# Optimization experiments

Hardware: AMD Instinct MI355X
Metric: run time of the kernel (lower is better)

## Reference

```python
import jax, jax.numpy as jnp
import numpy as np
from jax import lax

UNITS = [100, 80, 50, 30]
IN_FEAT = 64

def setup_inputs() -> dict:
    key = jax.random.key(0)
    ks = jax.random.split(key, 16)
    B, T, F = 512, 512, IN_FEAT
    ins = [F] + UNITS[:-1]
    d = {"x": jax.random.normal(ks[0], (B, T, F), jnp.float32)}
    for li, (u, fi) in enumerate(zip(UNITS, ins)):
        din = u + fi  # concat([h, x]) per the cell
        scale = 1.0 / np.sqrt(din)
        d[f"W{li}"] = jax.random.normal(ks[1 + li], (din, 4 * u), jnp.float32) * scale
        d[f"b{li}"] = jnp.zeros((4 * u,), jnp.float32)
    d["Wout"] = jax.random.normal(ks[10], (UNITS[-1], 1), jnp.float32) * (1.0 / np.sqrt(UNITS[-1]))
    d["bout"] = jnp.zeros((1,), jnp.float32)
    return d

def _lstm_layer(x, W, b, units, return_sequences):
    # x: [B, T, F] -> hidden sequence [B, T, units] or last hidden [B, units]
    B = x.shape[0]
    h0 = jnp.zeros((B, units), x.dtype)
    c0 = jnp.zeros((B, units), x.dtype)

    def step(carry, xt):
        h, c = carry
        z = jnp.concatenate([h, xt], axis=-1) @ W + b  # [B, 4u]
        f, i, g, o = jnp.split(z, 4, axis=-1)  # gate order: forget, input, candidate, output
        f = jax.nn.sigmoid(f)
        i = jax.nn.sigmoid(i)
        g = jnp.tanh(g)
        c_new = f * c + i * g
        h_new = jax.nn.sigmoid(o) * jnp.tanh(c_new)
        return (h_new, c_new), (h_new if return_sequences else None)

    xs = jnp.swapaxes(x, 0, 1)  # [T, B, F]
    (h_last, _), hs = lax.scan(step, (h0, c0), xs)
    if return_sequences:
        return jnp.swapaxes(hs, 0, 1)  # [B, T, units]
    return h_last

def reference(x, W0, b0, W1, b1, W2, b2, W3, b3, Wout, bout):
    # Dropout layers are identity at inference (training=False).
    h = _lstm_layer(x, W0, b0, UNITS[0], True)
    h = _lstm_layer(h, W1, b1, UNITS[1], True)
    h = _lstm_layer(h, W2, b2, UNITS[2], True)
    h = _lstm_layer(h, W3, b3, UNITS[3], False)  # last-layer RNN returns final hidden only
    return h @ Wout + bout  # [B, 1]
```

## Files before the change

### kernel.cpp

```cpp
#include <hip/hip_runtime.h>


#define T_SEQ 512
#define B_TOT 512

__device__ __forceinline__ float sigmoidf_(float x) {
    return 1.0f / (1.0f + __expf(-x));
}
__device__ __forceinline__ float tanh_fast(float x) {
    float e = __expf(2.0f * x);
    return 1.0f - 2.0f / (1.0f + e);
}

template<int U, int FI, int S, int JT, int BLOCK, int WEU, bool SEQ, bool FINAL>
__global__ __launch_bounds__(BLOCK, WEU)
void lstm_layer(const float* __restrict__ X,
                const float* __restrict__ W,
                const float* __restrict__ Bv,
                float* __restrict__ Hout,
                const float* __restrict__ Wd,
                const float* __restrict__ bd,
                float* __restrict__ OUT)
{
    constexpr int DIN  = U + FI;
    constexpr int DIN4 = ((DIN + 4*S - 1) / (4*S)) * (4*S);
    constexpr int KH   = DIN4 / S;
    constexpr int G    = 4 * U;
    constexpr int NP   = G / JT;
    constexpr int NT   = NP * S;

    __shared__ __align__(16) float in0[DIN4];
    __shared__ __align__(16) float in1[DIN4];
    __shared__ __align__(16) float zp[S * 2 * G];

    const int tid = threadIdx.x;
    const int bb  = blockIdx.x * 2;

    const int p = tid % NP;
    const int s = tid / NP;
    float w[JT][KH];
    if (tid < NT) {
        #pragma unroll
        for (int c = 0; c < JT; ++c) {
            #pragma unroll
            for (int kk = 0; kk < KH; ++kk) {
                const int k = s * KH + kk;
                w[c][kk] = (k < DIN) ? W[(size_t)k * G + (JT * p + c)] : 0.0f;
            }
        }
    }

    const int cb = (tid < 2*U) ? (tid / U) : 0;
    const int cu = (tid < 2*U) ? (tid - cb*U) : 0;
    float gbf = 0, gbi = 0, gbg = 0, gbo = 0, creg = 0.0f;
    if (tid < 2*U) {
        gbf = Bv[cu]; gbi = Bv[cu + U]; gbg = Bv[cu + 2*U]; gbo = Bv[cu + 3*U];
    }
    float* myin = cb ? in1 : in0;

    const int xb = (tid < 2*FI) ? (tid / FI) : 0;
    const int xk = (tid < 2*FI) ? (tid - xb*FI) : 0;
    const float* Xrow = X + (size_t)(bb + xb) * T_SEQ * FI + xk;
    float* xin = xb ? in1 : in0;

    for (int k = tid; k < DIN4; k += BLOCK) {
        if (k < U || k >= U + FI) { in0[k] = 0.0f; in1[k] = 0.0f; }
    }
    if (tid < 2*FI) xin[U + xk] = Xrow[0];
    __syncthreads();

    const float4* f40 = (const float4*)in0;
    const float4* f41 = (const float4*)in1;
    const int qbase = s * (KH / 4);

    for (int t = 0; t < T_SEQ; ++t) {
        float xpre = 0.0f;
        const bool do_x = (tid < 2*FI) && (t + 1 < T_SEQ);
        if (do_x) xpre = Xrow[(size_t)(t + 1) * FI];

        if (tid < NT) {
            float acc[JT][2];
            #pragma unroll
            for (int c = 0; c < JT; ++c) { acc[c][0] = 0.0f; acc[c][1] = 0.0f; }
            #pragma unroll
            for (int q = 0; q < KH/4; ++q) {
                const float4 av = f40[qbase + q];
                const float4 bv = f41[qbase + q];
                #pragma unroll
                for (int c = 0; c < JT; ++c) {
                    acc[c][0] += w[c][4*q+0] * av.x; acc[c][1] += w[c][4*q+0] * bv.x;
                    acc[c][0] += w[c][4*q+1] * av.y; acc[c][1] += w[c][4*q+1] * bv.y;
                    acc[c][0] += w[c][4*q+2] * av.z; acc[c][1] += w[c][4*q+2] * bv.z;
                    acc[c][0] += w[c][4*q+3] * av.w; acc[c][1] += w[c][4*q+3] * bv.w;
                }
            }
            float* z0 = &zp[(s*2 + 0) * G + JT * p];
            float* z1 = &zp[(s*2 + 1) * G + JT * p];
            #pragma unroll
            for (int c = 0; c < JT; ++c) { z0[c] = acc[c][0]; z1[c] = acc[c][1]; }
        }
        __syncthreads();

        if (tid < 2*U) {
            float zf = gbf, zi = gbi, zg = gbg, zo = gbo;
            #pragma unroll
            for (int s2 = 0; s2 < S; ++s2) {
                const float* zr = &zp[(s2*2 + cb) * G];
                zf += zr[cu]; zi += zr[cu + U]; zg += zr[cu + 2*U]; zo += zr[cu + 3*U];
            }
            const float fg = sigmoidf_(zf);
            const float ig = sigmoidf_(zi);
            const float gg = tanh_fast(zg);
            const float og = sigmoidf_(zo);
            creg = fg * creg + ig * gg;
            const float hn = og * tanh_fast(creg);
            myin[cu] = hn;
            if constexpr (SEQ) {
                Hout[((size_t)(bb + cb) * T_SEQ + t) * U + cu] = hn;
            }
        }
        if (do_x) xin[U + xk] = xpre;
        __syncthreads();
    }

    if constexpr (FINAL) {
        if (tid < 2) {
            const float* hh = tid ? in1 : in0;
            float acc = bd[0];
            #pragma unroll
            for (int u2 = 0; u2 < U; ++u2) acc += hh[u2] * Wd[u2];
            OUT[bb + tid] = acc;
        }
    }
}

extern "C" void kernel_launch(void* const* d_in, const int* in_sizes, int n_in,
                              void* d_out, int out_size, void* d_ws, size_t ws_size,
                              hipStream_t stream)
{
    const float* x    = (const float*)d_in[0];
    const float* W0   = (const float*)d_in[1];
    const float* b0   = (const float*)d_in[2];
    const float* W1   = (const float*)d_in[3];
    const float* b1   = (const float*)d_in[4];
    const float* W2   = (const float*)d_in[5];
    const float* b2   = (const float*)d_in[6];
    const float* W3   = (const float*)d_in[7];
    const float* b3   = (const float*)d_in[8];
    const float* Wout = (const float*)d_in[9];
    const float* bout = (const float*)d_in[10];
    float* out = (float*)d_out;

    float* H0 = (float*)d_ws;
    float* H1 = H0 + (size_t)B_TOT * T_SEQ * 100;
    float* H2 = (float*)d_ws;

    const dim3 grid(B_TOT / 2);

    hipLaunchKernelGGL((lstm_layer<100,  64, 4, 4, 448, 2, true,  false>),
                       grid, dim3(448), 0, stream, x,  W0, b0, H0, nullptr, nullptr, nullptr);
    hipLaunchKernelGGL((lstm_layer< 80, 100, 4, 2, 640, 3, true,  false>),
                       grid, dim3(640), 0, stream, H0, W1, b1, H1, nullptr, nullptr, nullptr);
    hipLaunchKernelGGL((lstm_layer< 50,  80, 4, 2, 448, 2, true,  false>),
                       grid, dim3(448), 0, stream, H1, W2, b2, H2, nullptr, nullptr, nullptr);
    hipLaunchKernelGGL((lstm_layer< 30,  50, 4, 2, 256, 2, false, true >),
                       grid, dim3(256), 0, stream, H2, W3, b3, nullptr, Wout, bout, out);
}
```

Before: 2.259 ms.

## Interleave batch rows in double-buffered LDS input and assign all four gates per thread

Stores the two batch rows' input vectors interleaved and double-buffered in shared memory, so each float4 load supplies two k values for both rows, and the next-step x write no longer needs a separate barrier phase. Each GEMV thread now owns one unit's four gates, so partial sums are written and reduced as float4. The k-split and block size per layer are retuned. The final dense layer is reduced from per-thread products held in registers. Per-thread register weight storage grows to 4*KH floats, which may lower occupancy or cause spills for the larger KH values.

```diff
diff --git a/kernel.cpp b/kernel.cpp
--- a/kernel.cpp
+++ b/kernel.cpp
@@ -12,8 +12,8 @@
     return 1.0f - 2.0f / (1.0f + e);
 }
 
-template<int U, int FI, int S, int JT, int BLOCK, int WEU, bool SEQ, bool FINAL>
-__global__ __launch_bounds__(BLOCK, WEU)
+template<int U, int FI, int S, int KH, int BLOCK, bool SEQ, bool FINAL>
+__global__ __launch_bounds__(BLOCK, 2)
 void lstm_layer(const float* __restrict__ X,
                 const float* __restrict__ W,
                 const float* __restrict__ Bv,
@@ -23,112 +23,115 @@
                 float* __restrict__ OUT)
 {
     constexpr int DIN  = U + FI;
-    constexpr int DIN4 = ((DIN + 4*S - 1) / (4*S)) * (4*S);
-    constexpr int KH   = DIN4 / S;
-    constexpr int G    = 4 * U;
-    constexpr int NP   = G / JT;
-    constexpr int NT   = NP * S;
+    constexpr int DIN4 = S * KH;
+    static_assert(DIN4 >= DIN, "k-padding must cover DIN");
+    static_assert((KH & 1) == 0, "KH even: one float4 = 2 k x 2 rows");
+    constexpr int G  = 4 * U;
+    constexpr int NT = S * U;
+    static_assert(NT <= BLOCK, "GEMV threads must fit");
+    static_assert(NT >= 2 * FI, "prefetch threads must be GEMV threads");
+    constexpr int TOT = 2 * DIN4;
 
-    __shared__ __align__(16) float in0[DIN4];
-    __shared__ __align__(16) float in1[DIN4];
-    __shared__ __align__(16) float zp[S * 2 * G];
+    __shared__ __align__(16) float buf[2][TOT];
+    __shared__ __align__(16) float zp[S * 2 * U * 4];
 
     const int tid = threadIdx.x;
     const int bb  = blockIdx.x * 2;
 
-    const int p = tid % NP;
-    const int s = tid / NP;
-    float w[JT][KH];
+    const int p = tid % U;
+    const int s = tid / U;
+
+    float w[4][KH];
     if (tid < NT) {
         #pragma unroll
-        for (int c = 0; c < JT; ++c) {
+        for (int g = 0; g < 4; ++g) {
             #pragma unroll
             for (int kk = 0; kk < KH; ++kk) {
                 const int k = s * KH + kk;
-                w[c][kk] = (k < DIN) ? W[(size_t)k * G + (JT * p + c)] : 0.0f;
+                w[g][kk] = (k < DIN) ? W[(size_t)k * G + g * U + p] : 0.0f;
             }
         }
     }
 
-    const int cb = (tid < 2*U) ? (tid / U) : 0;
-    const int cu = (tid < 2*U) ? (tid - cb*U) : 0;
-    float gbf = 0, gbi = 0, gbg = 0, gbo = 0, creg = 0.0f;
-    if (tid < 2*U) {
-        gbf = Bv[cu]; gbi = Bv[cu + U]; gbg = Bv[cu + 2*U]; gbo = Bv[cu + 3*U];
+    float cb4[4] = {0.f, 0.f, 0.f, 0.f};
+    if (tid < 2 * U) {
+        #pragma unroll
+        for (int g = 0; g < 4; ++g) cb4[g] = Bv[g * U + p];
     }
-    float* myin = cb ? in1 : in0;
+    float hreg = 0.0f, creg = 0.0f;
+    float wdreg = 0.0f;
+    if constexpr (FINAL) { if (tid < 2 * U) wdreg = Wd[p]; }
 
-    const int xb = (tid < 2*FI) ? (tid / FI) : 0;
-    const int xk = (tid < 2*FI) ? (tid - xb*FI) : 0;
-    const float* Xrow = X + (size_t)(bb + xb) * T_SEQ * FI + xk;
-    float* xin = xb ? in1 : in0;
+    const int xr = (tid < FI) ? 0 : 1;
+    const int xj = tid - xr * FI;
+    const float* Xrow = X + (size_t)(bb + xr) * T_SEQ * FI + xj;
+    const int xwi = 2 * (U + xj) + xr;
 
-    for (int k = tid; k < DIN4; k += BLOCK) {
-        if (k < U || k >= U + FI) { in0[k] = 0.0f; in1[k] = 0.0f; }
-    }
-    if (tid < 2*FI) xin[U + xk] = Xrow[0];
+    for (int i = tid; i < 2 * TOT; i += BLOCK) ((float*)buf)[i] = 0.0f;
+    __syncthreads();
+    if (tid < 2 * FI) buf[0][xwi] = Xrow[0];
     __syncthreads();
 
-    const float4* f40 = (const float4*)in0;
-    const float4* f41 = (const float4*)in1;
-    const int qbase = s * (KH / 4);
+    const int rbase = s * (KH / 2);
 
     for (int t = 0; t < T_SEQ; ++t) {
+        const int cur = t & 1, nxt = cur ^ 1;
+
         float xpre = 0.0f;
-        const bool do_x = (tid < 2*FI) && (t + 1 < T_SEQ);
+        const bool do_x = (tid < 2 * FI) && (t + 1 < T_SEQ);
         if (do_x) xpre = Xrow[(size_t)(t + 1) * FI];
 
         if (tid < NT) {
-            float acc[JT][2];
+            float a0 = 0.f, a1 = 0.f, a2 = 0.f, a3 = 0.f;
+            float b0 = 0.f, b1 = 0.f, b2 = 0.f, b3 = 0.f;
+            const float4* rb = (const float4*)buf[cur];
             #pragma unroll
-            for (int c = 0; c < JT; ++c) { acc[c][0] = 0.0f; acc[c][1] = 0.0f; }
-            #pragma unroll
-            for (int q = 0; q < KH/4; ++q) {
-                const float4 av = f40[qbase + q];
-                const float4 bv = f41[qbase + q];
-                #pragma unroll
-                for (int c = 0; c < JT; ++c) {
-                    acc[c][0] += w[c][4*q+0] * av.x; acc[c][1] += w[c][4*q+0] * bv.x;
-                    acc[c][0] += w[c][4*q+1] * av.y; acc[c][1] += w[c][4*q+1] * bv.y;
-                    acc[c][0] += w[c][4*q+2] * av.z; acc[c][1] += w[c][4*q+2] * bv.z;
-                    acc[c][0] += w[c][4*q+3] * av.w; acc[c][1] += w[c][4*q+3] * bv.w;
-                }
+            for (int q = 0; q < KH / 2; ++q) {
+                const float4 v = rb[rbase + q];
+                a0 += w[0][2*q] * v.x; b0 += w[0][2*q] * v.y;
+                a1 += w[1][2*q] * v.x; b1 += w[1][2*q] * v.y;
+                a2 += w[2][2*q] * v.x; b2 += w[2][2*q] * v.y;
+                a3 += w[3][2*q] * v.x; b3 += w[3][2*q] * v.y;
+                a0 += w[0][2*q+1] * v.z; b0 += w[0][2*q+1] * v.w;
+                a1 += w[1][2*q+1] * v.z; b1 += w[1][2*q+1] * v.w;
+                a2 += w[2][2*q+1] * v.z; b2 += w[2][2*q+1] * v.w;
+                a3 += w[3][2*q+1] * v.z; b3 += w[3][2*q+1] * v.w;
             }
-            float* z0 = &zp[(s*2 + 0) * G + JT * p];
-            float* z1 = &zp[(s*2 + 1) * G + JT * p];
-            #pragma unroll
-            for (int c = 0; c < JT; ++c) { z0[c] = acc[c][0]; z1[c] = acc[c][1]; }
+            float4* zq = (float4*)zp;
+            zq[(s * 2 + 0) * U + p] = make_float4(a0, a1, a2, a3);
+            zq[(s * 2 + 1) * U + p] = make_float4(b0, b1, b2, b3);
         }
+        if (do_x) buf[nxt][xwi] = xpre;
         __syncthreads();
 
-        if (tid < 2*U) {
-            float zf = gbf, zi = gbi, zg = gbg, zo = gbo;
+        if (tid < 2 * U) {
+            float z0 = cb4[0], z1 = cb4[1], z2 = cb4[2], z3 = cb4[3];
+            const float4* zq = (const float4*)zp;
             #pragma unroll
-            for (int s2 = 0; s2 < S; ++s2) {
-                const float* zr = &zp[(s2*2 + cb) * G];
-                zf += zr[cu]; zi += zr[cu + U]; zg += zr[cu + 2*U]; zo += zr[cu + 3*U];
+            for (int ss = 0; ss < S; ++ss) {
+                const float4 v = zq[(ss * 2 + s) * U + p];
+                z0 += v.x; z1 += v.y; z2 += v.z; z3 += v.w;
             }
-            const float fg = sigmoidf_(zf);
-            const float ig = sigmoidf_(zi);
-            const float gg = tanh_fast(zg);
-            const float og = sigmoidf_(zo);
-            creg = fg * creg + ig * gg;
-            const float hn = og * tanh_fast(creg);
-            myin[cu] = hn;
+            const float F  = sigmoidf_(z0);
+            const float I  = sigmoidf_(z1);
+            const float Gv = tanh_fast(z2);
+            const float O  = sigmoidf_(z3);
+            creg = F * creg + I * Gv;
+            hreg = O * tanh_fast(creg);
+            buf[nxt][2 * p + s] = hreg;
             if constexpr (SEQ) {
-                Hout[((size_t)(bb + cb) * T_SEQ + t) * U + cu] = hn;
+                Hout[((size_t)(bb + s) * T_SEQ + t) * U + p] = hreg;
             }
         }
-        if (do_x) xin[U + xk] = xpre;
         __syncthreads();
     }
 
     if constexpr (FINAL) {
+        if (tid < 2 * U) buf[0][2 * p + s] = hreg * wdreg;
+        __syncthreads();
         if (tid < 2) {
-            const float* hh = tid ? in1 : in0;
             float acc = bd[0];
-            #pragma unroll
-            for (int u2 = 0; u2 < U; ++u2) acc += hh[u2] * Wd[u2];
+            for (int u = 0; u < U; ++u) acc += buf[0][2 * u + tid];
             OUT[bb + tid] = acc;
         }
     }
@@ -157,12 +160,12 @@
 
     const dim3 grid(B_TOT / 2);
 
-    hipLaunchKernelGGL((lstm_layer<100,  64, 4, 4, 448, 2, true,  false>),
-                       grid, dim3(448), 0, stream, x,  W0, b0, H0, nullptr, nullptr, nullptr);
-    hipLaunchKernelGGL((lstm_layer< 80, 100, 4, 2, 640, 3, true,  false>),
-                       grid, dim3(640), 0, stream, H0, W1, b1, H1, nullptr, nullptr, nullptr);
-    hipLaunchKernelGGL((lstm_layer< 50,  80, 4, 2, 448, 2, true,  false>),
-                       grid, dim3(448), 0, stream, H1, W2, b2, H2, nullptr, nullptr, nullptr);
-    hipLaunchKernelGGL((lstm_layer< 30,  50, 4, 2, 256, 2, false, true >),
+    hipLaunchKernelGGL((lstm_layer<100,  64, 5, 36, 512, true,  false>),
+                       grid, dim3(512), 0, stream, x,  W0, b0, H0, nullptr, nullptr, nullptr);
+    hipLaunchKernelGGL((lstm_layer< 80, 100, 6, 30, 512, true,  false>),
+                       grid, dim3(512), 0, stream, H0, W1, b1, H1, nullptr, nullptr, nullptr);
+    hipLaunchKernelGGL((lstm_layer< 50,  80, 5, 26, 256, true,  false>),
+                       grid, dim3(256), 0, stream, H1, W2, b2, H2, nullptr, nullptr, nullptr);
+    hipLaunchKernelGGL((lstm_layer< 30,  50, 8, 10, 256, false, true >),
                        grid, dim3(256), 0, stream, H2, W3, b3, nullptr, Wout, bout, out);
 }
```

Result: faster. 1.955 ms (-13.5%).
